# Performance work log

Hardware: AMD Instinct MI355X
Metric: run time of the kernel (lower is better)

Reference implementation:

```python
import jax, jax.numpy as jnp
import numpy as np

GRID_SIZE = 5
SPLINE_ORDER = 3
INPUT_DIM = 4096
BATCH = 4096
N_BASIS = GRID_SIZE + SPLINE_ORDER - 1  # 7


def _extended_knots():
    # Uniform grid on [-1, 1] extended by spline_order knots on each side so the
    # Cox-de Boor recursion is well defined (the original torch code indexes
    # grid[i+k+1] past the end; this is the standard intended knot extension).
    grid = np.linspace(-1.0, 1.0, GRID_SIZE)
    h = grid[1] - grid[0]
    left = grid[0] - h * np.arange(SPLINE_ORDER, 0, -1)
    right = grid[-1] + h * np.arange(1, SPLINE_ORDER + 1)
    return jnp.asarray(np.concatenate([left, grid, right]), dtype=jnp.float32)  # (11,)


def _bspline_basis(x, knots):
    # x: (B, D) -> basis: (B, D, N_BASIS), fully vectorized Cox-de Boor recursion.
    t = knots
    xe = x[..., None]                                   # (B, D, 1)
    Bk = ((xe >= t[:-1]) & (xe < t[1:])).astype(x.dtype)  # degree 0: (B, D, 10)
    for k in range(1, SPLINE_ORDER + 1):
        n = t.shape[0] - k - 1
        left = (xe - t[:n]) / (t[k:k + n] - t[:n]) * Bk[..., :n]
        right = (t[k + 1:k + 1 + n] - xe) / (t[k + 1:k + 1 + n] - t[1:1 + n]) * Bk[..., 1:n + 1]
        Bk = left + right
    return Bk  # (B, D, 7)


def setup_inputs() -> dict:
    key = jax.random.key(0)
    kx, kc = jax.random.split(key)
    x = jax.random.uniform(kx, (BATCH, INPUT_DIM), dtype=jnp.float32, minval=-1.0, maxval=1.0)
    coeffs = jax.random.normal(kc, (INPUT_DIM, N_BASIS), dtype=jnp.float32)
    return {"x": x, "coeffs": coeffs}


def reference(x, coeffs):
    knots = _extended_knots()
    basis = _bspline_basis(x, knots)          # (B, D, K)
    return jnp.einsum('bdk,dk->bd', basis, coeffs)
```

## Files before the change

### kernel.cpp

```cpp
#include <hip/hip_runtime.h>


#define D     4096
#define B     4096
#define NB    7
#define DTILE 256
#define ROWS  64

constexpr int NDT    = D / DTILE;
constexpr int NRT    = B / ROWS;
constexpr int STRIDE = 20;

__global__ __launch_bounds__(256, 4) void
spline_act_kernel(const float* __restrict__ x,
                  const float* __restrict__ coeffs,
                  float* __restrict__ out) {
    __shared__ float sc[DTILE * STRIDE];

    const int bid   = blockIdx.x;
    const int dt    = bid & (NDT - 1);
    const int rowt  = bid >> 4;
    const int dbase = dt * DTILE;

    {
        const int i = threadIdx.x;
        const float* crow = coeffs + (size_t)(dbase + i) * NB;
        float c0 = crow[0], c1 = crow[1], c2 = crow[2], c3 = crow[3];
        float c4 = crow[4], c5 = crow[5], c6 = crow[6];
        float* bp = &sc[i * STRIDE];
        *reinterpret_cast<float4*>(bp + 0)  = make_float4(c0, c1, c2, c3);
        *reinterpret_cast<float4*>(bp + 4)  = make_float4(c1, c2, c3, c4);
        *reinterpret_cast<float4*>(bp + 8)  = make_float4(c2, c3, c4, c5);
        *reinterpret_cast<float4*>(bp + 12) = make_float4(c3, c4, c5, c6);
    }
    __syncthreads();

    const int tid  = threadIdx.x;
    const int pos  = tid & 63;
    const int rsub = tid >> 6;

    const float4* x4 = reinterpret_cast<const float4*>(x);
    float4*       o4 = reinterpret_cast<float4*>(out);

    const int rowbase = rowt * ROWS;
    const int colbase = (dbase >> 2) + pos;
    const float k6 = 1.0f / 6.0f;

#pragma unroll
    for (int g = 0; g < ROWS / 16; ++g) {
        float4 xv[4];
        int    idx[4];
#pragma unroll
        for (int it = 0; it < 4; ++it) {
            int row = rowbase + (g * 4 + it) * 4 + rsub;
            idx[it] = row * (D / 4) + colbase;
            xv[it]  = x4[idx[it]];
        }
#pragma unroll
        for (int it = 0; it < 4; ++it) {
            float xs[4] = {xv[it].x, xv[it].y, xv[it].z, xv[it].w};
            float r[4];
#pragma unroll
            for (int j = 0; j < 4; ++j) {
                float u = (xs[j] + 1.0f) * 2.0f;
                int c = (int)u;
                c = c > 3 ? 3 : c;
                float s = u - (float)c;

                float s2  = s * s;
                float s3  = s2 * s;
                float omt = 1.0f - s;
                float w0 = omt * omt * omt * k6;
                float w1 = (3.0f * s3 - 6.0f * s2 + 4.0f) * k6;
                float w2 = (-3.0f * s3 + 3.0f * s2 + 3.0f * s + 1.0f) * k6;
                float w3 = s3 * k6;

                int dl = 4 * pos + j;
                float4 cv = *reinterpret_cast<const float4*>(&sc[dl * STRIDE + 4 * c]);
                r[j] = w0 * cv.x + w1 * cv.y + w2 * cv.z + w3 * cv.w;
            }
            o4[idx[it]] = make_float4(r[0], r[1], r[2], r[3]);
        }
    }
}

extern "C" void kernel_launch(void* const* d_in, const int* in_sizes, int n_in,
                              void* d_out, int out_size, void* d_ws, size_t ws_size,
                              hipStream_t stream) {
    const float* x      = (const float*)d_in[0];
    const float* coeffs = (const float*)d_in[1];
    float* out          = (float*)d_out;

    const int grid = NDT * NRT;
    spline_act_kernel<<<grid, 256, 0, stream>>>(x, coeffs, out);
}
```

Before: 116.1 us.

## Precompute per-interval cubic polynomial coefficients in registers, drop shared memory

Each thread now owns four fixed columns and converts their B-spline coefficients into power-basis cubic polynomial coefficients for each of the four intervals, held in 64 registers. The evaluation becomes a select plus a Horner chain in place of computing the basis weights and reading coefficients from shared memory. This removes the LDS table, the block barrier and the per-element shared reads. The tile shape changes to 1024 columns by 8 rows, so each block streams fewer rows against more columns, and register pressure rises sharply, which may reduce occupancy.

New measurement: 127.0 us. 9.4% more time.

```diff
diff --git a/kernel.cpp b/kernel.cpp
--- a/kernel.cpp
+++ b/kernel.cpp
@@ -4,56 +4,53 @@
 #define D     4096
 #define B     4096
 #define NB    7
-#define DTILE 256
-#define ROWS  64
+#define DTILE 1024
+#define ROWS  8
 
-constexpr int NDT    = D / DTILE;
-constexpr int NRT    = B / ROWS;
-constexpr int STRIDE = 20;
+constexpr int NDT = D / DTILE;
+constexpr int NRT = B / ROWS;
 
 __global__ __launch_bounds__(256, 4) void
 spline_act_kernel(const float* __restrict__ x,
                   const float* __restrict__ coeffs,
                   float* __restrict__ out) {
-    __shared__ float sc[DTILE * STRIDE];
-
     const int bid   = blockIdx.x;
     const int dt    = bid & (NDT - 1);
-    const int rowt  = bid >> 4;
+    const int rowt  = bid >> 2;
     const int dbase = dt * DTILE;
+    const int tid   = threadIdx.x;
 
-    {
-        const int i = threadIdx.x;
-        const float* crow = coeffs + (size_t)(dbase + i) * NB;
-        float c0 = crow[0], c1 = crow[1], c2 = crow[2], c3 = crow[3];
-        float c4 = crow[4], c5 = crow[5], c6 = crow[6];
-        float* bp = &sc[i * STRIDE];
-        *reinterpret_cast<float4*>(bp + 0)  = make_float4(c0, c1, c2, c3);
-        *reinterpret_cast<float4*>(bp + 4)  = make_float4(c1, c2, c3, c4);
-        *reinterpret_cast<float4*>(bp + 8)  = make_float4(c2, c3, c4, c5);
-        *reinterpret_cast<float4*>(bp + 12) = make_float4(c3, c4, c5, c6);
+    const int d0 = dbase + 4 * tid;
+
+    float pa0[4][4], pa1[4][4], pa2[4][4], pa3[4][4];
+#pragma unroll
+    for (int col = 0; col < 4; ++col) {
+        const float* cr = coeffs + (size_t)(d0 + col) * NB;
+        float tap[NB];
+#pragma unroll
+        for (int k = 0; k < NB; ++k) tap[k] = cr[k];
+#pragma unroll
+        for (int c = 0; c < 4; ++c) {
+            float cA = tap[c], cB = tap[c + 1], cC = tap[c + 2], cD = tap[c + 3];
+            pa0[col][c] = (cA + 4.0f * cB + cC) * (1.0f / 6.0f);
+            pa1[col][c] = (cC - cA) * 0.5f;
+            pa2[col][c] = (cA - 2.0f * cB + cC) * 0.5f;
+            pa3[col][c] = ((cD - cA) + 3.0f * (cB - cC)) * (1.0f / 6.0f);
+        }
     }
-    __syncthreads();
-
-    const int tid  = threadIdx.x;
-    const int pos  = tid & 63;
-    const int rsub = tid >> 6;
 
     const float4* x4 = reinterpret_cast<const float4*>(x);
     float4*       o4 = reinterpret_cast<float4*>(out);
-
+    const int colbase = (dbase >> 2) + tid;
     const int rowbase = rowt * ROWS;
-    const int colbase = (dbase >> 2) + pos;
-    const float k6 = 1.0f / 6.0f;
 
 #pragma unroll
-    for (int g = 0; g < ROWS / 16; ++g) {
+    for (int g = 0; g < ROWS / 4; ++g) {
         float4 xv[4];
         int    idx[4];
 #pragma unroll
         for (int it = 0; it < 4; ++it) {
-            int row = rowbase + (g * 4 + it) * 4 + rsub;
-            idx[it] = row * (D / 4) + colbase;
+            idx[it] = (rowbase + g * 4 + it) * (D / 4) + colbase;
             xv[it]  = x4[idx[it]];
         }
 #pragma unroll
@@ -62,22 +59,19 @@
             float r[4];
 #pragma unroll
             for (int j = 0; j < 4; ++j) {
-                float u = (xs[j] + 1.0f) * 2.0f;
+                float u = fmaf(xs[j], 2.0f, 2.0f);
                 int c = (int)u;
                 c = c > 3 ? 3 : c;
                 float s = u - (float)c;
 
-                float s2  = s * s;
-                float s3  = s2 * s;
-                float omt = 1.0f - s;
-                float w0 = omt * omt * omt * k6;
-                float w1 = (3.0f * s3 - 6.0f * s2 + 4.0f) * k6;
-                float w2 = (-3.0f * s3 + 3.0f * s2 + 3.0f * s + 1.0f) * k6;
-                float w3 = s3 * k6;
+                bool hi = c >= 2;
+                bool lo = (c & 1) != 0;
+                float q0 = hi ? (lo ? pa0[j][3] : pa0[j][2]) : (lo ? pa0[j][1] : pa0[j][0]);
+                float q1 = hi ? (lo ? pa1[j][3] : pa1[j][2]) : (lo ? pa1[j][1] : pa1[j][0]);
+                float q2 = hi ? (lo ? pa2[j][3] : pa2[j][2]) : (lo ? pa2[j][1] : pa2[j][0]);
+                float q3 = hi ? (lo ? pa3[j][3] : pa3[j][2]) : (lo ? pa3[j][1] : pa3[j][0]);
 
-                int dl = 4 * pos + j;
-                float4 cv = *reinterpret_cast<const float4*>(&sc[dl * STRIDE + 4 * c]);
-                r[j] = w0 * cv.x + w1 * cv.y + w2 * cv.z + w3 * cv.w;
+                r[j] = fmaf(s, fmaf(s, fmaf(s, q3, q2), q1), q0);
             }
             o4[idx[it]] = make_float4(r[0], r[1], r[2], r[3]);
         }
```
